# Kernel tuning notes

Hardware: AMD Instinct MI355X
Metric: run time of the kernel (lower is better)

## Reference

```python
import jax, jax.numpy as jnp
import numpy as np

N_BATCHES = 32
FEAT = 32
NUM_BESSEL = 8
HID = 8
DIST = 5.0
EPS = 1e-6


def setup_inputs() -> dict:
    N, F, B, NB, H = 50000, FEAT, NUM_BESSEL, N_BATCHES, HID
    key = jax.random.key(0)
    k = jax.random.split(key, 16)
    pos = jax.random.normal(k[0], (N, 3), jnp.float32) * 10.0
    batch = jnp.sort(jax.random.randint(k[1], (N,), 0, NB)).astype(jnp.int32)
    node_features = jax.random.normal(k[2], (N, F), jnp.float32)
    bessel_weights = jnp.arange(1, B + 1, dtype=jnp.float32) * jnp.pi

    def w(kk, shape, fan):
        return jax.random.normal(kk, shape, jnp.float32) / np.sqrt(fan).astype(np.float32)

    return dict(
        pos=pos, batch=batch, node_features=node_features,
        bessel_weights=bessel_weights,
        W_q_dummy=w(k[3], (F, F), F),
        Wk_gen1=w(k[4], (B, H), B), Wk_gen2=w(k[5], (H, F * F), H),
        Wv_gen1=w(k[6], (B, H), B), Wv_gen2=w(k[7], (H, F * F), H),
        W_q_graph=w(k[8], (F, F), F),
        Wkg_gen1=w(k[9], (B, H), B), Wkg_gen2=w(k[10], (H, F * F), H),
        Wvg_gen1=w(k[11], (B, H), B), Wvg_gen2=w(k[12], (H, F * F), H),
        W_dot=w(k[13], (F, F), F),
        init_dummy=jax.random.normal(k[14], (F,), jnp.float32),
    )


def _bessel(x, bw):
    # BesselBasisNoCutoff: sin(n*pi*x)/(x+eps), x: (N,) -> (N, B)
    return jnp.sin(bw * x[..., None]) / (x[..., None] + EPS)


def _gen_weights(edge_emb, W1, W2, F):
    # FullyConnectedNet([B, H, F*F], silu): (N,2,B) -> (N,2,F,F)
    h = jax.nn.silu(edge_emb @ W1)
    return (h @ W2).reshape(edge_emb.shape[0], 2, F, F)


def reference(pos, batch, node_features, bessel_weights,
              W_q_dummy, Wk_gen1, Wk_gen2, Wv_gen1, Wv_gen2,
              W_q_graph, Wkg_gen1, Wkg_gen2, Wvg_gen1, Wvg_gen2,
              W_dot, init_dummy):
    F = FEAT
    NB = N_BATCHES
    inv_sqrtF = 1.0 / np.sqrt(F).astype(np.float32)

    # ---- dummy edge features (Bessel basis on distance to top/bottom z surface) ----
    z = pos[:, 2]
    z_min = jax.ops.segment_min(z, batch, num_segments=NB, indices_are_sorted=True)
    z_max = jax.ops.segment_max(z, batch, num_segments=NB, indices_are_sorted=True)
    bottom_len = z - z_min[batch] + DIST          # (N,)
    top_len = z_max[batch] + DIST - z             # (N,)
    edge_emb = jnp.stack([_bessel(bottom_len, bessel_weights),
                          _bessel(top_len, bessel_weights)], axis=1)  # (N,2,B)
    # lmax=0 spherical harmonics, component normalization -> constant scalar 1

    # ---- dummy-node update: attention dummy(query) <- graph nodes (key/value) ----
    dummy_features = jnp.broadcast_to(init_dummy, (NB, 2, F))          # (NB,2,F)
    q_dummy = (dummy_features @ W_q_dummy) * inv_sqrtF                 # (NB,2,F)
    qn = q_dummy[batch]                                                # (N,2,F)

    Wk = _gen_weights(edge_emb, Wk_gen1, Wk_gen2, F)                   # (N,2,F,F)
    Wv = _gen_weights(edge_emb, Wv_gen1, Wv_gen2, F)
    k_d = jnp.einsum('nf,nsfg->nsg', node_features, Wk) * inv_sqrtF    # (N,2,F)
    v_d = jnp.einsum('nf,nsfg->nsg', node_features, Wv) * inv_sqrtF

    # dot: FullyConnectedTensorProduct(q, k -> 0e), scaled by 1/sqrt(scale_dim)
    scores = jnp.einsum('nsf,nsg,fg->ns', qn, k_d, W_dot) / F * inv_sqrtF  # (N,2)

    # per-batch softmax over graph nodes (segment softmax)
    smax = jax.ops.segment_max(scores, batch, num_segments=NB, indices_are_sorted=True)
    ex = jnp.exp(scores - smax[batch])
    denom = jax.ops.segment_sum(ex, batch, num_segments=NB, indices_are_sorted=True)
    attn = ex / denom[batch]                                           # (N,2)
    agg = jax.ops.segment_sum(attn[..., None] * v_d, batch,
                              num_segments=NB, indices_are_sorted=True)  # (NB,2,F)
    dummy_out = dummy_features + agg

    # ---- graph-node update: attention node(query) <- 2 dummy nodes (key/value) ----
    q_g = (node_features @ W_q_graph) * inv_sqrtF                      # (N,F)
    Wkg = _gen_weights(edge_emb, Wkg_gen1, Wkg_gen2, F)                # (N,2,F,F)
    Wvg = _gen_weights(edge_emb, Wvg_gen1, Wvg_gen2, F)
    d_per_node = dummy_out[batch]                                      # (N,2,F)
    k_g = jnp.einsum('nsf,nsfg->nsg', d_per_node, Wkg) * inv_sqrtF
    v_g = jnp.einsum('nsf,nsfg->nsg', d_per_node, Wvg) * inv_sqrtF
    scores_g = jnp.einsum('nf,nsg,fg->ns', q_g, k_g, W_dot) / F * inv_sqrtF  # (N,2)
    attn_g = jax.nn.softmax(scores_g, axis=1)
    node_out = node_features + jnp.einsum('ns,nsf->nf', attn_g, v_g)
    return node_out, dummy_out
```

## Files before the change

### kernel.cpp

```cpp
#include <hip/hip_runtime.h>

#define NBATCH 32
#define DIST 5.0f
#define EPSV 1e-6f
#define INV_SQRT_F 0.17677669529663687f
#define SC_STAGE2 1.72633492e-4f
#define SL1 7
#define SL2 7

__device__ __forceinline__ float silu_f(float v) { return __fdividef(v, 1.0f + __expf(-v)); }

__device__ __forceinline__ unsigned f2key(float f) {
  unsigned u = __float_as_uint(f);
  return (u & 0x80000000u) ? ~u : (u | 0x80000000u);
}
__device__ __forceinline__ float key2f(unsigned k) {
  return (k & 0x80000000u) ? __uint_as_float(k ^ 0x80000000u) : __uint_as_float(~k);
}

extern "C" __global__ __launch_bounds__(256)
void prep_kernel(const float* __restrict__ pos, const int* __restrict__ batch,
                 const float* __restrict__ Wqd, const float* __restrict__ Wdot,
                 const float* __restrict__ Wqg, const float* __restrict__ Wk2,
                 const float* __restrict__ initd,
                 unsigned* __restrict__ ws_zp,
                 int* __restrict__ ws_seg,
                 float* __restrict__ ws_Mk,
                 float* __restrict__ ws_WQD,
                 int N, int ZT)
{
  const int blk = blockIdx.x, tid = threadIdx.x;
  if (blk < ZT) {
    __shared__ unsigned s_pmin[NBATCH], s_pmax[NBATCH];
    if (tid < NBATCH) { s_pmin[tid] = 0xFFFFFFFFu; s_pmax[tid] = 0u; }
    __syncthreads();
    int i = (blk << 8) + tid;
    if (i < N) {
      int b = batch[i];
      unsigned k = f2key(pos[3 * (size_t)i + 2]);
      atomicMin(&s_pmin[b], k);
      atomicMax(&s_pmax[b], k);
      int bp = (i == 0) ? -1 : batch[i - 1];
      for (int bb = bp + 1; bb <= b; bb++) ws_seg[bb] = i;
      if (i == N - 1) for (int bb = b + 1; bb <= NBATCH; bb++) ws_seg[bb] = N;
    }
    __syncthreads();
    if (tid < NBATCH) {
      ws_zp[blk * 64 + tid]      = s_pmin[tid];
      ws_zp[blk * 64 + 32 + tid] = s_pmax[tid];
    }
  } else if (blk == ZT) {
    __shared__ float s_q[32], s_c[32];
    if (tid < 32) {
      float a = 0.f;
      #pragma unroll
      for (int f = 0; f < 32; f++) a += initd[f] * Wqd[f * 32 + tid];
      s_q[tid] = a * INV_SQRT_F;
    }
    __syncthreads();
    if (tid < 32) {
      float a = 0.f;
      #pragma unroll
      for (int f = 0; f < 32; f++) a += s_q[f] * Wdot[f * 32 + tid];
      s_c[tid] = a;
    }
    __syncthreads();
    {
      int f = tid >> 3, h = tid & 7;
      const float* w = &Wk2[h * 1024 + f * 32];
      float a = 0.f;
      #pragma unroll
      for (int g = 0; g < 32; g++) a += w[g] * s_c[g];
      ws_Mk[tid] = a * (1.0f / 1024.0f);
    }
  } else {
    for (int idx = tid; idx < 1024; idx += 256) {
      int f = idx >> 5, g = idx & 31;
      float a = 0.f;
      #pragma unroll
      for (int k = 0; k < 32; k++) a += Wqg[f * 32 + k] * Wdot[k * 32 + g];
      ws_WQD[idx] = a;
    }
  }
}

extern "C" __global__ __launch_bounds__(256)
void stage1_kernel(const float* __restrict__ pos,
                   const float* __restrict__ xfeat,
                   const float* __restrict__ bw,
                   const float* __restrict__ Wk1,
                   const float* __restrict__ Wv1,
                   const int*   __restrict__ ws_seg,
                   const unsigned* __restrict__ ws_zp,
                   const float* __restrict__ ws_Mk,
                   float* __restrict__ ws_Tp,
                   float* __restrict__ ws_denp,
                   float* __restrict__ ws_zf,
                   int N, int ZT)
{
  const int b = blockIdx.x / SL1, jb = blockIdx.x % SL1;
  const int tid = threadIdx.x;

  __shared__ unsigned s_ru[256];
  __shared__ float s_red[256];
  __shared__ float s_bw[8];
  __shared__ float s_Wa[8][8], s_Wb[8][8];
  __shared__ float s_Mk[32][8];
  __shared__ float s_exh[256][17];
  __shared__ float s_xs[256][36];
  __shared__ float s_Tp[4][512];

  unsigned kmn = 0xFFFFFFFFu, kmx = 0u;
  for (int t = tid; t < ZT; t += 256) {
    kmn = min(kmn, ws_zp[t * 64 + b]);
    kmx = max(kmx, ws_zp[t * 64 + 32 + b]);
  }
  s_ru[tid] = kmn; __syncthreads();
  for (int off = 128; off > 0; off >>= 1) { if (tid < off) s_ru[tid] = min(s_ru[tid], s_ru[tid + off]); __syncthreads(); }
  const unsigned rmn = s_ru[0]; __syncthreads();
  s_ru[tid] = kmx; __syncthreads();
  for (int off = 128; off > 0; off >>= 1) { if (tid < off) s_ru[tid] = max(s_ru[tid], s_ru[tid + off]); __syncthreads(); }
  const unsigned rmx = s_ru[0];
  const float zmin = key2f(rmn), zmax = key2f(rmx);

  if (tid < 8) s_bw[tid] = bw[tid];
  if (tid < 64) { s_Wa[tid >> 3][tid & 7] = Wk1[tid]; s_Wb[tid >> 3][tid & 7] = Wv1[tid]; }
  s_Mk[tid >> 3][tid & 7] = ws_Mk[tid];
  const int ss0 = ws_seg[b], ss1 = ws_seg[b + 1];
  __syncthreads();

  const int cnt = ss1 - ss0;
  const int per = (cnt + SL1 - 1) / SL1;
  const int lo = ss0 + jb * per;
  const int hi = min(lo + per, ss1);

  float Treg[8] = {0,0,0,0,0,0,0,0};
  float d0 = 0.f, d1 = 0.f;
  const int group = tid >> 6, gt = tid & 63, osh = gt >> 2, ofg = gt & 3;

  for (int base = lo; base < hi; base += 256) {
    int i = base + tid;
    if (i < hi) {
      float z = pos[3 * (size_t)i + 2];
      float len0 = z - zmin + DIST, len1 = zmax + DIST - z;
      float xv[32];
      const float4* xp = (const float4*)&xfeat[(size_t)i * 32];
      float4* xso = (float4*)s_xs[tid];
      #pragma unroll
      for (int q = 0; q < 8; q++) {
        float4 t = xp[q];
        xso[q] = t;
        xv[4*q] = t.x; xv[4*q+1] = t.y; xv[4*q+2] = t.z; xv[4*q+3] = t.w;
      }
      float u[8] = {0,0,0,0,0,0,0,0};
      #pragma unroll
      for (int f = 0; f < 32; f++) {
        float xf = xv[f];
        #pragma unroll
        for (int h = 0; h < 8; h++) u[h] += xf * s_Mk[f][h];
      }
      #pragma unroll
      for (int s = 0; s < 2; s++) {
        float L = s ? len1 : len0;
        float inv = __fdividef(1.0f, L + EPSV);
        float ee[8];
        #pragma unroll
        for (int j = 0; j < 8; j++) ee[j] = __sinf(s_bw[j] * L) * inv;
        float sc = 0.f;
        #pragma unroll
        for (int h = 0; h < 8; h++) {
          float a = 0.f;
          #pragma unroll
          for (int j = 0; j < 8; j++) a += ee[j] * s_Wa[j][h];
          sc += silu_f(a) * u[h];
        }
        float ex = __expf(fminf(fmaxf(sc, -60.f), 60.f));
        if (s) d1 += ex; else d0 += ex;
        #pragma unroll
        for (int h = 0; h < 8; h++) {
          float v = 0.f;
          #pragma unroll
          for (int j = 0; j < 8; j++) v += ee[j] * s_Wb[j][h];
          s_exh[tid][8*s + h] = ex * silu_f(v);
        }
      }
    } else {
      #pragma unroll
      for (int h = 0; h < 16; h++) s_exh[tid][h] = 0.f;
      float4* xso = (float4*)s_xs[tid];
      float4 z4 = make_float4(0.f, 0.f, 0.f, 0.f);
      #pragma unroll
      for (int q = 0; q < 8; q++) xso[q] = z4;
    }
    __syncthreads();
    const int cb = group * 64;
    for (int c = cb; c < cb + 64; c++) {
      float eh = s_exh[c][osh];
      const float4* xr4 = (const float4*)&s_xs[c][ofg * 8];
      float4 xa = xr4[0], xb = xr4[1];
      Treg[0] += eh * xa.x; Treg[1] += eh * xa.y; Treg[2] += eh * xa.z; Treg[3] += eh * xa.w;
      Treg[4] += eh * xb.x; Treg[5] += eh * xb.y; Treg[6] += eh * xb.z; Treg[7] += eh * xb.w;
    }
    __syncthreads();
  }
  #pragma unroll
  for (int k = 0; k < 8; k++) s_Tp[group][osh * 32 + ofg * 8 + k] = Treg[k];
  __syncthreads();
  const int slot = b * SL1 + jb;
  for (int idx = tid; idx < 512; idx += 256)
    ws_Tp[slot * 512 + idx] = s_Tp[0][idx] + s_Tp[1][idx] + s_Tp[2][idx] + s_Tp[3][idx];
  s_red[tid] = d0; __syncthreads();
  for (int off = 128; off > 0; off >>= 1) { if (tid < off) s_red[tid] += s_red[tid + off]; __syncthreads(); }
  if (tid == 0) ws_denp[slot * 2 + 0] = s_red[0];
  __syncthreads();
  s_red[tid] = d1; __syncthreads();
  for (int off = 128; off > 0; off >>= 1) { if (tid < off) s_red[tid] += s_red[tid + off]; __syncthreads(); }
  if (tid == 0) ws_denp[slot * 2 + 1] = s_red[0];
  if (jb == 0 && tid == 0) { ws_zf[2*b] = zmin; ws_zf[2*b+1] = zmax; }
}

extern "C" __global__ __launch_bounds__(256)
void stage2_kernel(const float* __restrict__ pos,
                   const float* __restrict__ xfeat,
                   const float* __restrict__ bw,
                   const float* __restrict__ Wkg1, const float* __restrict__ Wkg2,
                   const float* __restrict__ Wvg1, const float* __restrict__ Wvg2,
                   const float* __restrict__ Wv2,  const float* __restrict__ initd,
                   const int*   __restrict__ ws_seg,
                   const float* __restrict__ ws_Tp,
                   const float* __restrict__ ws_denp,
                   const float* __restrict__ ws_zf,
                   const float* __restrict__ ws_WQD,
                   float* __restrict__ out_node, float* __restrict__ out_dummy,
                   int N)
{
  const int b = blockIdx.x / SL2, jb = blockIdx.x % SL2;
  const int tid = threadIdx.x;

  __shared__ float s_bw[8];
  __shared__ float s_Wa[8][8], s_Wb[8][8];
  __shared__ float s_T[512];
  __shared__ float s_den[2];
  __shared__ float s_dp[4][2][32];
  __shared__ float s_dm[2][32];
  __shared__ float s_WQD[32][32];
  __shared__ float s_Bkg[16][32];
  __shared__ float s_Bvg[16][32];
  __shared__ float s_G[32][16];

  if (tid < 8) s_bw[tid] = bw[tid];
  if (tid < 64) { s_Wa[tid >> 3][tid & 7] = Wkg1[tid]; s_Wb[tid >> 3][tid & 7] = Wvg1[tid]; }
  if (tid < 2) {
    float d = 0.f;
    #pragma unroll
    for (int j = 0; j < SL1; j++) d += ws_denp[(b * SL1 + j) * 2 + tid];
    s_den[tid] = d;
  }
  for (int idx = tid; idx < 512; idx += 256) {
    float a = 0.f;
    #pragma unroll
    for (int j = 0; j < SL1; j++) a += ws_Tp[(b * SL1 + j) * 512 + idx];
    s_T[idx] = a;
  }
  for (int idx = tid; idx < 1024; idx += 256) s_WQD[idx >> 5][idx & 31] = ws_WQD[idx];
  const float zmin = ws_zf[2*b], zmax = ws_zf[2*b+1];
  const int ss0 = ws_seg[b], ss1 = ws_seg[b + 1];
  __syncthreads();

  {
    int g = tid & 31, s = (tid >> 5) & 1, fq = tid >> 6;
    float acc = 0.f;
    #pragma unroll
    for (int h = 0; h < 8; h++) {
      #pragma unroll
      for (int f8 = 0; f8 < 8; f8++) {
        int f = fq * 8 + f8;
        acc += s_T[(8 * s + h) * 32 + f] * Wv2[h * 1024 + f * 32 + g];
      }
    }
    s_dp[fq][s][g] = acc;
  }
  __syncthreads();
  if (tid < 64) {
    int s = tid >> 5, g = tid & 31;
    float acc = s_dp[0][s][g] + s_dp[1][s][g] + s_dp[2][s][g] + s_dp[3][s][g];
    float dn = s_den[s];
    float dv = initd[g] + (dn > 0.f ? acc * INV_SQRT_F * __fdividef(1.0f, dn) : 0.f);
    s_dm[s][g] = dv;
    if (jb == 0) out_dummy[b * 64 + tid] = dv;
  }
  __syncthreads();
  for (int idx = tid; idx < 512; idx += 256) {
    int sh = idx >> 5, g = idx & 31, s = sh >> 3, h = sh & 7;
    const float* wk = &Wkg2[h * 1024 + g];
    const float* wv = &Wvg2[h * 1024 + g];
    float a = 0.f, v = 0.f;
    #pragma unroll
    for (int f = 0; f < 32; f++) { float d = s_dm[s][f]; a += d * wk[f * 32]; v += d * wv[f * 32]; }
    s_Bkg[sh][g] = a;
    s_Bvg[sh][g] = v;
  }
  __syncthreads();
  for (int idx = tid; idx < 512; idx += 256) {
    int f = idx >> 4, sh = idx & 15;
    float a = 0.f;
    #pragma unroll
    for (int g = 0; g < 32; g++) a += s_WQD[f][g] * s_Bkg[sh][g];
    s_G[f][sh] = a * SC_STAGE2;
  }
  __syncthreads();

  const int cnt = ss1 - ss0;
  const int per = (cnt + SL2 - 1) / SL2;
  const int lo = ss0 + tid + jb * per;
  const int hi = min(ss0 + (jb + 1) * per, ss1);

  for (int i = lo; i < hi; i += 256) {
    float z = pos[3 * (size_t)i + 2];
    float len0 = z - zmin + DIST, len1 = zmax + DIST - z;
    float ee[16];
    #pragma unroll
    for (int s = 0; s < 2; s++) {
      float L = s ? len1 : len0;
      float inv = __fdividef(1.0f, L + EPSV);
      #pragma unroll
      for (int j = 0; j < 8; j++) ee[8*s + j] = __sinf(s_bw[j] * L) * inv;
    }
    float hkg[16], hvg[16];
    #pragma unroll
    for (int s = 0; s < 2; s++) {
      #pragma unroll
      for (int h = 0; h < 8; h++) {
        float a = 0.f, v = 0.f;
        #pragma unroll
        for (int j = 0; j < 8; j++) { a += ee[8*s + j] * s_Wa[j][h]; v += ee[8*s + j] * s_Wb[j][h]; }
        hkg[8*s + h] = silu_f(a); hvg[8*s + h] = silu_f(v);
      }
    }
    float xv[32];
    const float4* xp = (const float4*)&xfeat[(size_t)i * 32];
    #pragma unroll
    for (int q = 0; q < 8; q++) { float4 t = xp[q]; xv[4*q] = t.x; xv[4*q+1] = t.y; xv[4*q+2] = t.z; xv[4*q+3] = t.w; }
    float ev[16] = {0,0,0,0,0,0,0,0,0,0,0,0,0,0,0,0};
    #pragma unroll
    for (int f = 0; f < 32; f++) {
      float xf = xv[f];
      #pragma unroll
      for (int sh = 0; sh < 16; sh++) ev[sh] += xf * s_G[f][sh];
    }
    float sc0 = 0.f, sc1 = 0.f;
    #pragma unroll
    for (int h = 0; h < 8; h++) { sc0 += hkg[h] * ev[h]; sc1 += hkg[8 + h] * ev[8 + h]; }
    float m = fmaxf(sc0, sc1);
    float a0 = __expf(sc0 - m), a1 = __expf(sc1 - m);
    float invd = __fdividef(1.0f, a0 + a1);
    float w0 = a0 * invd * INV_SQRT_F, w1 = a1 * invd * INV_SQRT_F;
    float wv[16];
    #pragma unroll
    for (int sh = 0; sh < 16; sh++) wv[sh] = (sh < 8 ? w0 : w1) * hvg[sh];
    float ov[32];
    #pragma unroll
    for (int g = 0; g < 32; g++) ov[g] = xv[g];
    #pragma unroll
    for (int sh = 0; sh < 16; sh++) {
      float w = wv[sh];
      #pragma unroll
      for (int g = 0; g < 32; g++) ov[g] += w * s_Bvg[sh][g];
    }
    float4* op = (float4*)&out_node[(size_t)i * 32];
    #pragma unroll
    for (int q = 0; q < 8; q++) op[q] = make_float4(ov[4*q], ov[4*q+1], ov[4*q+2], ov[4*q+3]);
  }
}

extern "C" void kernel_launch(void* const* d_in, const int* in_sizes, int n_in,
                              void* d_out, int out_size, void* d_ws, size_t ws_size,
                              hipStream_t stream)
{
  const float* pos   = (const float*)d_in[0];
  const int*   batch = (const int*)d_in[1];
  const float* xf    = (const float*)d_in[2];
  const float* bw    = (const float*)d_in[3];
  const float* Wqd   = (const float*)d_in[4];
  const float* Wk1   = (const float*)d_in[5];
  const float* Wk2   = (const float*)d_in[6];
  const float* Wv1   = (const float*)d_in[7];
  const float* Wv2   = (const float*)d_in[8];
  const float* Wqg   = (const float*)d_in[9];
  const float* Wkg1  = (const float*)d_in[10];
  const float* Wkg2  = (const float*)d_in[11];
  const float* Wvg1  = (const float*)d_in[12];
  const float* Wvg2  = (const float*)d_in[13];
  const float* Wdot  = (const float*)d_in[14];
  const float* initd = (const float*)d_in[15];
  int N = in_sizes[1];

  float* out_node  = (float*)d_out;
  float* out_dummy = out_node + (size_t)N * 32;

  float*    ws      = (float*)d_ws;
  float*    ws_Tp   = ws;
  float*    ws_denp = ws + 114688;
  float*    ws_zf   = ws + 115200;
  int*      ws_seg  = (int*)(ws + 115264);
  float*    ws_Mk   = ws + 115312;
  float*    ws_WQD  = ws + 115568;
  unsigned* ws_zp   = (unsigned*)(ws + 116592);

  const int ZT = (N + 255) >> 8;

  prep_kernel<<<ZT + 2, 256, 0, stream>>>(pos, batch, Wqd, Wdot, Wqg, Wk2, initd,
                                          ws_zp, ws_seg, ws_Mk, ws_WQD, N, ZT);

  stage1_kernel<<<NBATCH * SL1, 256, 0, stream>>>(pos, xf, bw, Wk1, Wv1, ws_seg, ws_zp,
                                                  ws_Mk, ws_Tp, ws_denp, ws_zf, N, ZT);

  stage2_kernel<<<NBATCH * SL2, 256, 0, stream>>>(pos, xf, bw, Wkg1, Wkg2, Wvg1, Wvg2,
                                                  Wv2, initd, ws_seg, ws_Tp, ws_denp,
                                                  ws_zf, ws_WQD, out_node, out_dummy, N);
}
```

Measured before the change: 45.75 us.

## Fold prep kernel into stage kernels using binary-search segment bounds

Removes the separate prep kernel launch. Each stage1 block now finds its segment bounds by binary search over the sorted batch array, computes the z min/max of its segment directly, and recomputes the small Mk weight products locally. Stage2 recomputes the Wqg·Wdot matrix per block and also binary-searches its segment bounds. This drops one launch and one global round trip, at the cost of redundant per-block work: each of the 7 slices per batch rescans that batch's z values and recomputes the weight products.

After: 46.56 us. Within noise of the previous version (+1.8%).

```diff
diff --git a/kernel.cpp b/kernel.cpp
--- a/kernel.cpp
+++ b/kernel.cpp
@@ -18,85 +18,27 @@
   return (k & 0x80000000u) ? __uint_as_float(k ^ 0x80000000u) : __uint_as_float(~k);
 }
 
-extern "C" __global__ __launch_bounds__(256)
-void prep_kernel(const float* __restrict__ pos, const int* __restrict__ batch,
-                 const float* __restrict__ Wqd, const float* __restrict__ Wdot,
-                 const float* __restrict__ Wqg, const float* __restrict__ Wk2,
-                 const float* __restrict__ initd,
-                 unsigned* __restrict__ ws_zp,
-                 int* __restrict__ ws_seg,
-                 float* __restrict__ ws_Mk,
-                 float* __restrict__ ws_WQD,
-                 int N, int ZT)
-{
-  const int blk = blockIdx.x, tid = threadIdx.x;
-  if (blk < ZT) {
-    __shared__ unsigned s_pmin[NBATCH], s_pmax[NBATCH];
-    if (tid < NBATCH) { s_pmin[tid] = 0xFFFFFFFFu; s_pmax[tid] = 0u; }
-    __syncthreads();
-    int i = (blk << 8) + tid;
-    if (i < N) {
-      int b = batch[i];
-      unsigned k = f2key(pos[3 * (size_t)i + 2]);
-      atomicMin(&s_pmin[b], k);
-      atomicMax(&s_pmax[b], k);
-      int bp = (i == 0) ? -1 : batch[i - 1];
-      for (int bb = bp + 1; bb <= b; bb++) ws_seg[bb] = i;
-      if (i == N - 1) for (int bb = b + 1; bb <= NBATCH; bb++) ws_seg[bb] = N;
-    }
-    __syncthreads();
-    if (tid < NBATCH) {
-      ws_zp[blk * 64 + tid]      = s_pmin[tid];
-      ws_zp[blk * 64 + 32 + tid] = s_pmax[tid];
-    }
-  } else if (blk == ZT) {
-    __shared__ float s_q[32], s_c[32];
-    if (tid < 32) {
-      float a = 0.f;
-      #pragma unroll
-      for (int f = 0; f < 32; f++) a += initd[f] * Wqd[f * 32 + tid];
-      s_q[tid] = a * INV_SQRT_F;
-    }
-    __syncthreads();
-    if (tid < 32) {
-      float a = 0.f;
-      #pragma unroll
-      for (int f = 0; f < 32; f++) a += s_q[f] * Wdot[f * 32 + tid];
-      s_c[tid] = a;
-    }
-    __syncthreads();
-    {
-      int f = tid >> 3, h = tid & 7;
-      const float* w = &Wk2[h * 1024 + f * 32];
-      float a = 0.f;
-      #pragma unroll
-      for (int g = 0; g < 32; g++) a += w[g] * s_c[g];
-      ws_Mk[tid] = a * (1.0f / 1024.0f);
-    }
-  } else {
-    for (int idx = tid; idx < 1024; idx += 256) {
-      int f = idx >> 5, g = idx & 31;
-      float a = 0.f;
-      #pragma unroll
-      for (int k = 0; k < 32; k++) a += Wqg[f * 32 + k] * Wdot[k * 32 + g];
-      ws_WQD[idx] = a;
-    }
-  }
+__device__ __forceinline__ int lower_bound_i(const int* __restrict__ batch, int N, int key) {
+  int lo = 0, hi = N;
+  while (lo < hi) { int m = (lo + hi) >> 1; if (batch[m] < key) lo = m + 1; else hi = m; }
+  return lo;
 }
 
 extern "C" __global__ __launch_bounds__(256)
 void stage1_kernel(const float* __restrict__ pos,
+                   const int*   __restrict__ batch,
                    const float* __restrict__ xfeat,
                    const float* __restrict__ bw,
+                   const float* __restrict__ Wqd,
                    const float* __restrict__ Wk1,
+                   const float* __restrict__ Wk2,
                    const float* __restrict__ Wv1,
-                   const int*   __restrict__ ws_seg,
-                   const unsigned* __restrict__ ws_zp,
-                   const float* __restrict__ ws_Mk,
+                   const float* __restrict__ Wdot,
+                   const float* __restrict__ initd,
                    float* __restrict__ ws_Tp,
                    float* __restrict__ ws_denp,
                    float* __restrict__ ws_zf,
-                   int N, int ZT)
+                   int N)
 {
   const int b = blockIdx.x / SL1, jb = blockIdx.x % SL1;
   const int tid = threadIdx.x;
@@ -104,16 +46,44 @@
   __shared__ unsigned s_ru[256];
   __shared__ float s_red[256];
   __shared__ float s_bw[8];
+  __shared__ float s_q[32], s_c[32];
   __shared__ float s_Wa[8][8], s_Wb[8][8];
   __shared__ float s_Mk[32][8];
   __shared__ float s_exh[256][17];
   __shared__ float s_xs[256][36];
   __shared__ float s_Tp[4][512];
 
+  if (tid < 8) s_bw[tid] = bw[tid];
+  if (tid < 64) { s_Wa[tid >> 3][tid & 7] = Wk1[tid]; s_Wb[tid >> 3][tid & 7] = Wv1[tid]; }
+  if (tid < 32) {
+    float a = 0.f;
+    #pragma unroll
+    for (int f = 0; f < 32; f++) a += initd[f] * Wqd[f * 32 + tid];
+    s_q[tid] = a * INV_SQRT_F;
+  }
+  const int ss0 = lower_bound_i(batch, N, b);
+  const int ss1 = lower_bound_i(batch, N, b + 1);
+  __syncthreads();
+  if (tid < 32) {
+    float a = 0.f;
+    #pragma unroll
+    for (int f = 0; f < 32; f++) a += s_q[f] * Wdot[f * 32 + tid];
+    s_c[tid] = a;
+  }
+  __syncthreads();
+  {
+    int f = tid >> 3, h = tid & 7;
+    const float* w = &Wk2[h * 1024 + f * 32];
+    float a = 0.f;
+    #pragma unroll
+    for (int g = 0; g < 32; g++) a += w[g] * s_c[g];
+    s_Mk[f][h] = a * (1.0f / 1024.0f);
+  }
+
   unsigned kmn = 0xFFFFFFFFu, kmx = 0u;
-  for (int t = tid; t < ZT; t += 256) {
-    kmn = min(kmn, ws_zp[t * 64 + b]);
-    kmx = max(kmx, ws_zp[t * 64 + 32 + b]);
+  for (int i = ss0 + tid; i < ss1; i += 256) {
+    unsigned k = f2key(pos[3 * (size_t)i + 2]);
+    kmn = min(kmn, k); kmx = max(kmx, k);
   }
   s_ru[tid] = kmn; __syncthreads();
   for (int off = 128; off > 0; off >>= 1) { if (tid < off) s_ru[tid] = min(s_ru[tid], s_ru[tid + off]); __syncthreads(); }
@@ -121,13 +91,8 @@
   s_ru[tid] = kmx; __syncthreads();
   for (int off = 128; off > 0; off >>= 1) { if (tid < off) s_ru[tid] = max(s_ru[tid], s_ru[tid + off]); __syncthreads(); }
   const unsigned rmx = s_ru[0];
+  __syncthreads();
   const float zmin = key2f(rmn), zmax = key2f(rmx);
-
-  if (tid < 8) s_bw[tid] = bw[tid];
-  if (tid < 64) { s_Wa[tid >> 3][tid & 7] = Wk1[tid]; s_Wb[tid >> 3][tid & 7] = Wv1[tid]; }
-  s_Mk[tid >> 3][tid & 7] = ws_Mk[tid];
-  const int ss0 = ws_seg[b], ss1 = ws_seg[b + 1];
-  __syncthreads();
 
   const int cnt = ss1 - ss0;
   const int per = (cnt + SL1 - 1) / SL1;
@@ -221,16 +186,16 @@
 
 extern "C" __global__ __launch_bounds__(256)
 void stage2_kernel(const float* __restrict__ pos,
+                   const int*   __restrict__ batch,
                    const float* __restrict__ xfeat,
                    const float* __restrict__ bw,
+                   const float* __restrict__ Wqg,  const float* __restrict__ Wdot,
                    const float* __restrict__ Wkg1, const float* __restrict__ Wkg2,
                    const float* __restrict__ Wvg1, const float* __restrict__ Wvg2,
                    const float* __restrict__ Wv2,  const float* __restrict__ initd,
-                   const int*   __restrict__ ws_seg,
                    const float* __restrict__ ws_Tp,
                    const float* __restrict__ ws_denp,
                    const float* __restrict__ ws_zf,
-                   const float* __restrict__ ws_WQD,
                    float* __restrict__ out_node, float* __restrict__ out_dummy,
                    int N)
 {
@@ -262,9 +227,16 @@
     for (int j = 0; j < SL1; j++) a += ws_Tp[(b * SL1 + j) * 512 + idx];
     s_T[idx] = a;
   }
-  for (int idx = tid; idx < 1024; idx += 256) s_WQD[idx >> 5][idx & 31] = ws_WQD[idx];
+  for (int idx = tid; idx < 1024; idx += 256) {
+    int f = idx >> 5, g = idx & 31;
+    float a = 0.f;
+    #pragma unroll
+    for (int k = 0; k < 32; k++) a += Wqg[f * 32 + k] * Wdot[k * 32 + g];
+    s_WQD[f][g] = a;
+  }
+  const int ss0 = lower_bound_i(batch, N, b);
+  const int ss1 = lower_bound_i(batch, N, b + 1);
   const float zmin = ws_zf[2*b], zmax = ws_zf[2*b+1];
-  const int ss0 = ws_seg[b], ss1 = ws_seg[b + 1];
   __syncthreads();
 
   {
@@ -398,24 +370,15 @@
   float* out_node  = (float*)d_out;
   float* out_dummy = out_node + (size_t)N * 32;
 
-  float*    ws      = (float*)d_ws;
-  float*    ws_Tp   = ws;
-  float*    ws_denp = ws + 114688;
-  float*    ws_zf   = ws + 115200;
-  int*      ws_seg  = (int*)(ws + 115264);
-  float*    ws_Mk   = ws + 115312;
-  float*    ws_WQD  = ws + 115568;
-  unsigned* ws_zp   = (unsigned*)(ws + 116592);
-
-  const int ZT = (N + 255) >> 8;
-
-  prep_kernel<<<ZT + 2, 256, 0, stream>>>(pos, batch, Wqd, Wdot, Wqg, Wk2, initd,
-                                          ws_zp, ws_seg, ws_Mk, ws_WQD, N, ZT);
-
-  stage1_kernel<<<NBATCH * SL1, 256, 0, stream>>>(pos, xf, bw, Wk1, Wv1, ws_seg, ws_zp,
-                                                  ws_Mk, ws_Tp, ws_denp, ws_zf, N, ZT);
-
-  stage2_kernel<<<NBATCH * SL2, 256, 0, stream>>>(pos, xf, bw, Wkg1, Wkg2, Wvg1, Wvg2,
-                                                  Wv2, initd, ws_seg, ws_Tp, ws_denp,
-                                                  ws_zf, ws_WQD, out_node, out_dummy, N);
-}
+  float* ws      = (float*)d_ws;
+  float* ws_Tp   = ws;
+  float* ws_denp = ws + 114688;
+  float* ws_zf   = ws + 115200;
+
+  stage1_kernel<<<NBATCH * SL1, 256, 0, stream>>>(pos, batch, xf, bw, Wqd, Wk1, Wk2, Wv1,
+                                                  Wdot, initd, ws_Tp, ws_denp, ws_zf, N);
+
+  stage2_kernel<<<NBATCH * SL2, 256, 0, stream>>>(pos, batch, xf, bw, Wqg, Wdot, Wkg1, Wkg2,
+                                                  Wvg1, Wvg2, Wv2, initd, ws_Tp, ws_denp,
+                                                  ws_zf, out_node, out_dummy, N);
+}
```
